# Kernel optimization log

Measured on AMD Instinct MI355X. Metric: run time of the kernel, lower is better.

The kernel has to match this reference:

```python
import jax, jax.numpy as jnp
import numpy as np

N_NODES = 100000
N_EDGES = 6400000
DIM_FEAT = 5


def setup_inputs() -> dict:
    key = jax.random.key(0)
    k1, k2, k3 = jax.random.split(key, 3)
    features = jax.random.normal(k1, (N_NODES, DIM_FEAT), dtype=jnp.float32)
    src = jax.random.randint(k2, (N_EDGES,), 0, N_NODES, dtype=jnp.int64)
    dst = jax.random.randint(k3, (N_EDGES,), 0, N_NODES, dtype=jnp.int64)
    return {"features": features, "src": src, "dst": dst}


def reference(features, src, dst):
    # copy_u('h','m') then sum('m','h'):
    # h_out[v] = sum over edges (u->v) of features[u]
    msgs = features[src]  # [E, F] gather
    h = jax.ops.segment_sum(msgs, dst, num_segments=N_NODES)  # [N, F]
    return h
```

## Files before the change

### kernel.cpp

```cpp
#include <hip/hip_runtime.h>
#include <hip/hip_bf16.h>


#define NN     100000
#define FD     5
#define NOUTT  (NN * FD)
#define NPS    128
#define NPS_SH 7
#define NB     782
#define NBP    1024
#define NSB    256
#define BLK    256

__global__ __launch_bounds__(BLK) void k1_pad(const float* __restrict__ f,
                                              float4* __restrict__ fp) {
    int i = blockIdx.x * BLK + threadIdx.x;
    if (i < NN) {
        const float* r = f + (long long)i * FD;
        fp[2 * i]     = make_float4(r[0], r[1], r[2], r[3]);
        fp[2 * i + 1] = make_float4(r[4], 0.f, 0.f, 0.f);
    }
}

__global__ __launch_bounds__(BLK) void k2_hist(const int* __restrict__ dst,
                                               int* __restrict__ blk_hist, int chunk) {
    __shared__ int h[NB];
    for (int b = threadIdx.x; b < NB; b += BLK) h[b] = 0;
    __syncthreads();
    long long e0 = (long long)blockIdx.x * chunk;
    const int4* d4 = (const int4*)(dst + e0);
    int n4 = chunk >> 2;
    for (int i = threadIdx.x; i < n4; i += BLK) {
        int4 d = d4[i];
        atomicAdd(&h[d.x >> NPS_SH], 1);
        atomicAdd(&h[d.y >> NPS_SH], 1);
        atomicAdd(&h[d.z >> NPS_SH], 1);
        atomicAdd(&h[d.w >> NPS_SH], 1);
    }
    __syncthreads();
    for (int b = threadIdx.x; b < NB; b += BLK)
        blk_hist[b * NSB + blockIdx.x] = h[b];
}

__global__ __launch_bounds__(BLK) void k3_scanblk(int* __restrict__ blk_hist,
                                                  int* __restrict__ btot) {
    __shared__ int s[BLK];
    int b = blockIdx.x, t = threadIdx.x;
    int x = blk_hist[b * NSB + t];
    s[t] = x;
    __syncthreads();
    for (int off = 1; off < BLK; off <<= 1) {
        int v = (t >= off) ? s[t - off] : 0;
        __syncthreads();
        s[t] += v;
        __syncthreads();
    }
    blk_hist[b * NSB + t] = s[t] - x;
    if (t == BLK - 1) btot[b] = s[t];
}

__global__ __launch_bounds__(BLK) void k4_scanbkt(const int* __restrict__ btot,
                                                  int* __restrict__ bbase) {
    __shared__ int s[BLK];
    int t = threadIdx.x;
    int v[4], sum = 0;
#pragma unroll
    for (int k = 0; k < 4; ++k) {
        int i = 4 * t + k;
        v[k] = (i < NB) ? btot[i] : 0;
        sum += v[k];
    }
    s[t] = sum;
    __syncthreads();
    for (int off = 1; off < BLK; off <<= 1) {
        int u = (t >= off) ? s[t - off] : 0;
        __syncthreads();
        s[t] += u;
        __syncthreads();
    }
    int run = s[t] - sum;
#pragma unroll
    for (int k = 0; k < 4; ++k) { bbase[4 * t + k] = run; run += v[k]; }
}

__global__ __launch_bounds__(BLK) void k5_scatter(const int* __restrict__ src,
                                                  const int* __restrict__ dst,
                                                  const int* __restrict__ blk_hist,
                                                  const int* __restrict__ bbase,
                                                  int* __restrict__ bdata, int chunk) {
    __shared__ int cur[NB];
    int blk = blockIdx.x;
    for (int b = threadIdx.x; b < NB; b += BLK)
        cur[b] = bbase[b] + blk_hist[b * NSB + blk];
    __syncthreads();
    long long e0 = (long long)blk * chunk;
    const int4* d4 = (const int4*)(dst + e0);
    const int4* s4 = (const int4*)(src + e0);
    int n4 = chunk >> 2;
    for (int i = threadIdx.x; i < n4; i += BLK) {
        int4 d = d4[i];
        int4 s = s4[i];
        int vv[4] = {d.x, d.y, d.z, d.w};
        int uu[4] = {s.x, s.y, s.z, s.w};
#pragma unroll
        for (int j = 0; j < 4; ++j) {
            int b = vv[j] >> NPS_SH;
            int off = atomicAdd(&cur[b], 1);
            bdata[off] = (uu[j] << NPS_SH) | (vv[j] & (NPS - 1));
        }
    }
}

__global__ __launch_bounds__(BLK) void k6_gather(const int* __restrict__ bdata,
                                                 const float4* __restrict__ fp,
                                                 const int* __restrict__ bbase,
                                                 const int* __restrict__ btot,
                                                 float* __restrict__ out) {
    __shared__ float acc[NPS * FD];
    for (int j = threadIdx.x; j < NPS * FD; j += BLK) acc[j] = 0.f;
    __syncthreads();
    int b = blockIdx.x;
    int base = bbase[b];
    int n = btot[b];
    int t = threadIdx.x;
    int i = t;
    for (; i + 3 * BLK < n; i += 4 * BLK) {
        int w0 = bdata[base + i];
        int w1 = bdata[base + i + BLK];
        int w2 = bdata[base + i + 2 * BLK];
        int w3 = bdata[base + i + 3 * BLK];
        int u0 = w0 >> NPS_SH, l0 = w0 & (NPS - 1);
        int u1 = w1 >> NPS_SH, l1 = w1 & (NPS - 1);
        int u2 = w2 >> NPS_SH, l2 = w2 & (NPS - 1);
        int u3 = w3 >> NPS_SH, l3 = w3 & (NPS - 1);
        float4 a0 = fp[2 * u0], c0 = fp[2 * u0 + 1];
        float4 a1 = fp[2 * u1], c1 = fp[2 * u1 + 1];
        float4 a2 = fp[2 * u2], c2 = fp[2 * u2 + 1];
        float4 a3 = fp[2 * u3], c3 = fp[2 * u3 + 1];
        atomicAdd(&acc[l0 * FD + 0], a0.x); atomicAdd(&acc[l0 * FD + 1], a0.y);
        atomicAdd(&acc[l0 * FD + 2], a0.z); atomicAdd(&acc[l0 * FD + 3], a0.w);
        atomicAdd(&acc[l0 * FD + 4], c0.x);
        atomicAdd(&acc[l1 * FD + 0], a1.x); atomicAdd(&acc[l1 * FD + 1], a1.y);
        atomicAdd(&acc[l1 * FD + 2], a1.z); atomicAdd(&acc[l1 * FD + 3], a1.w);
        atomicAdd(&acc[l1 * FD + 4], c1.x);
        atomicAdd(&acc[l2 * FD + 0], a2.x); atomicAdd(&acc[l2 * FD + 1], a2.y);
        atomicAdd(&acc[l2 * FD + 2], a2.z); atomicAdd(&acc[l2 * FD + 3], a2.w);
        atomicAdd(&acc[l2 * FD + 4], c2.x);
        atomicAdd(&acc[l3 * FD + 0], a3.x); atomicAdd(&acc[l3 * FD + 1], a3.y);
        atomicAdd(&acc[l3 * FD + 2], a3.z); atomicAdd(&acc[l3 * FD + 3], a3.w);
        atomicAdd(&acc[l3 * FD + 4], c3.x);
    }
    for (; i < n; i += BLK) {
        int w = bdata[base + i];
        int u = w >> NPS_SH, l = w & (NPS - 1);
        float4 a = fp[2 * u], c = fp[2 * u + 1];
        atomicAdd(&acc[l * FD + 0], a.x); atomicAdd(&acc[l * FD + 1], a.y);
        atomicAdd(&acc[l * FD + 2], a.z); atomicAdd(&acc[l * FD + 3], a.w);
        atomicAdd(&acc[l * FD + 4], c.x);
    }
    __syncthreads();
    int node0 = b * NPS;
    int nn = NN - node0; if (nn > NPS) nn = NPS;
    int nfl = nn * FD;
    float* o = out + (long long)node0 * FD;
    for (int j = t; j < nfl; j += BLK) o[j] = acc[j];
}

__global__ void scatter_add_fallback(const float* __restrict__ features,
                                     const int* __restrict__ src,
                                     const int* __restrict__ dst,
                                     float* __restrict__ out, int n_edges) {
    int idx = blockIdx.x * blockDim.x + threadIdx.x;
    int stride = gridDim.x * blockDim.x;
    for (int e = idx; e < n_edges; e += stride) {
        int u = src[e], v = dst[e];
        const float* f = features + (long long)u * FD;
        float* o = out + (long long)v * FD;
#pragma unroll
        for (int k = 0; k < FD; ++k) atomicAdd(&o[k], f[k]);
    }
}

extern "C" void kernel_launch(void* const* d_in, const int* in_sizes, int n_in,
                              void* d_out, int out_size, void* d_ws, size_t ws_size,
                              hipStream_t stream) {
    const float* features = (const float*)d_in[0];
    const int*   src      = (const int*)d_in[1];
    const int*   dst      = (const int*)d_in[2];
    float* out = (float*)d_out;
    int n_edges = in_sizes[1];

    size_t o_bd = 0;
    size_t o_fp = o_bd + (size_t)n_edges * 4;
    size_t o_bh = o_fp + (size_t)NN * 2 * sizeof(float4);
    size_t o_bb = o_bh + (size_t)NB * NSB * 4;
    size_t o_bt = o_bb + (size_t)NBP * 4;
    size_t need = o_bt + (size_t)NBP * 4;

    bool fast = (out_size == NOUTT) && (in_sizes[0] == NOUTT) &&
                (n_edges % (NSB * 4) == 0) && (need <= ws_size);

    if (fast) {
        char* w = (char*)d_ws;
        int*    bdata = (int*)(w + o_bd);
        float4* fpad  = (float4*)(w + o_fp);
        int*    bhist = (int*)(w + o_bh);
        int*    bbase = (int*)(w + o_bb);
        int*    btot  = (int*)(w + o_bt);
        int chunk = n_edges / NSB;
        k1_pad   <<<(NN + BLK - 1) / BLK, BLK, 0, stream>>>(features, fpad);
        k2_hist  <<<NSB, BLK, 0, stream>>>(dst, bhist, chunk);
        k3_scanblk<<<NB, BLK, 0, stream>>>(bhist, btot);
        k4_scanbkt<<<1,  BLK, 0, stream>>>(btot, bbase);
        k5_scatter<<<NSB, BLK, 0, stream>>>(src, dst, bhist, bbase, bdata, chunk);
        k6_gather <<<NB,  BLK, 0, stream>>>(bdata, fpad, bbase, btot, out);
    } else {
        hipMemsetAsync(d_out, 0, (size_t)out_size * sizeof(float), stream);
        int grid = (n_edges + BLK - 1) / BLK;
        if (grid > 65535) grid = 65535;
        scatter_add_fallback<<<grid, BLK, 0, stream>>>(features, src, dst, out, n_edges);
    }
}
```

Baseline: 387.7 us.

## Shrink buckets to 32 nodes, 16-bit histograms, overlap pad buffer, deeper gather unroll

Reduces bucket size from 128 to 32 nodes (3125 buckets) and doubles the number of scatter blocks to 512. Per-block histograms are stored as row-major unsigned shorts, and the scan handles two entries per thread. The padded-feature buffer now reuses the histogram workspace, with the pad kernel moved after the scatter. The gather loop is unrolled 8 deep and loads only the needed fifth float. Smaller buckets and more blocks are meant to raise gather parallelism, and the smaller histogram cuts traffic, but the scan and scatter stages carry more per-bucket overhead, and the 16-bit counts rely on per-block bucket counts fitting in 16 bits.

```diff
diff --git a/kernel.cpp b/kernel.cpp
--- a/kernel.cpp
+++ b/kernel.cpp
@@ -5,25 +5,15 @@
 #define NN     100000
 #define FD     5
 #define NOUTT  (NN * FD)
-#define NPS    128
-#define NPS_SH 7
-#define NB     782
-#define NBP    1024
-#define NSB    256
+#define NPS    32
+#define NPS_SH 5
+#define NB     3125
+#define NSB    512
 #define BLK    256
 
-__global__ __launch_bounds__(BLK) void k1_pad(const float* __restrict__ f,
-                                              float4* __restrict__ fp) {
-    int i = blockIdx.x * BLK + threadIdx.x;
-    if (i < NN) {
-        const float* r = f + (long long)i * FD;
-        fp[2 * i]     = make_float4(r[0], r[1], r[2], r[3]);
-        fp[2 * i + 1] = make_float4(r[4], 0.f, 0.f, 0.f);
-    }
-}
-
 __global__ __launch_bounds__(BLK) void k2_hist(const int* __restrict__ dst,
-                                               int* __restrict__ blk_hist, int chunk) {
+                                               unsigned short* __restrict__ bh,
+                                               int chunk) {
     __shared__ int h[NB];
     for (int b = threadIdx.x; b < NB; b += BLK) h[b] = 0;
     __syncthreads();
@@ -38,16 +28,18 @@
         atomicAdd(&h[d.w >> NPS_SH], 1);
     }
     __syncthreads();
-    for (int b = threadIdx.x; b < NB; b += BLK)
-        blk_hist[b * NSB + blockIdx.x] = h[b];
-}
-
-__global__ __launch_bounds__(BLK) void k3_scanblk(int* __restrict__ blk_hist,
+    unsigned short* row = bh + (size_t)blockIdx.x * NB;
+    for (int b = threadIdx.x; b < NB; b += BLK) row[b] = (unsigned short)h[b];
+}
+
+__global__ __launch_bounds__(BLK) void k3_scanblk(unsigned short* __restrict__ bh,
                                                   int* __restrict__ btot) {
     __shared__ int s[BLK];
     int b = blockIdx.x, t = threadIdx.x;
-    int x = blk_hist[b * NSB + t];
-    s[t] = x;
+    int v0 = bh[(size_t)(2 * t)     * NB + b];
+    int v1 = bh[(size_t)(2 * t + 1) * NB + b];
+    int pair = v0 + v1;
+    s[t] = pair;
     __syncthreads();
     for (int off = 1; off < BLK; off <<= 1) {
         int v = (t >= off) ? s[t - off] : 0;
@@ -55,18 +47,21 @@
         s[t] += v;
         __syncthreads();
     }
-    blk_hist[b * NSB + t] = s[t] - x;
+    int base = s[t] - pair;
+    bh[(size_t)(2 * t)     * NB + b] = (unsigned short)base;
+    bh[(size_t)(2 * t + 1) * NB + b] = (unsigned short)(base + v0);
     if (t == BLK - 1) btot[b] = s[t];
 }
 
+#define VPT 13
 __global__ __launch_bounds__(BLK) void k4_scanbkt(const int* __restrict__ btot,
                                                   int* __restrict__ bbase) {
     __shared__ int s[BLK];
     int t = threadIdx.x;
-    int v[4], sum = 0;
-#pragma unroll
-    for (int k = 0; k < 4; ++k) {
-        int i = 4 * t + k;
+    int v[VPT], sum = 0;
+#pragma unroll
+    for (int k = 0; k < VPT; ++k) {
+        int i = VPT * t + k;
         v[k] = (i < NB) ? btot[i] : 0;
         sum += v[k];
     }
@@ -80,18 +75,23 @@
     }
     int run = s[t] - sum;
 #pragma unroll
-    for (int k = 0; k < 4; ++k) { bbase[4 * t + k] = run; run += v[k]; }
+    for (int k = 0; k < VPT; ++k) {
+        int i = VPT * t + k;
+        if (i < NB) bbase[i] = run;
+        run += v[k];
+    }
 }
 
 __global__ __launch_bounds__(BLK) void k5_scatter(const int* __restrict__ src,
                                                   const int* __restrict__ dst,
-                                                  const int* __restrict__ blk_hist,
+                                                  const unsigned short* __restrict__ bh,
                                                   const int* __restrict__ bbase,
                                                   int* __restrict__ bdata, int chunk) {
     __shared__ int cur[NB];
     int blk = blockIdx.x;
+    const unsigned short* row = bh + (size_t)blk * NB;
     for (int b = threadIdx.x; b < NB; b += BLK)
-        cur[b] = bbase[b] + blk_hist[b * NSB + blk];
+        cur[b] = bbase[b] + (int)row[b];
     __syncthreads();
     long long e0 = (long long)blk * chunk;
     const int4* d4 = (const int4*)(dst + e0);
@@ -111,59 +111,67 @@
     }
 }
 
+__global__ __launch_bounds__(BLK) void k1_pad(const float* __restrict__ f,
+                                              float4* __restrict__ fp) {
+    int i = blockIdx.x * BLK + threadIdx.x;
+    if (i < NN) {
+        const float* r = f + (long long)i * FD;
+        fp[2 * i]     = make_float4(r[0], r[1], r[2], r[3]);
+        fp[2 * i + 1] = make_float4(r[4], 0.f, 0.f, 0.f);
+    }
+}
+
+#define UNR 8
 __global__ __launch_bounds__(BLK) void k6_gather(const int* __restrict__ bdata,
                                                  const float4* __restrict__ fp,
                                                  const int* __restrict__ bbase,
                                                  const int* __restrict__ btot,
                                                  float* __restrict__ out) {
     __shared__ float acc[NPS * FD];
-    for (int j = threadIdx.x; j < NPS * FD; j += BLK) acc[j] = 0.f;
+    int t = threadIdx.x;
+    if (t < NPS * FD) acc[t] = 0.f;
     __syncthreads();
     int b = blockIdx.x;
     int base = bbase[b];
     int n = btot[b];
-    int t = threadIdx.x;
+    const float* fpf = (const float*)fp;
+
     int i = t;
-    for (; i + 3 * BLK < n; i += 4 * BLK) {
-        int w0 = bdata[base + i];
-        int w1 = bdata[base + i + BLK];
-        int w2 = bdata[base + i + 2 * BLK];
-        int w3 = bdata[base + i + 3 * BLK];
-        int u0 = w0 >> NPS_SH, l0 = w0 & (NPS - 1);
-        int u1 = w1 >> NPS_SH, l1 = w1 & (NPS - 1);
-        int u2 = w2 >> NPS_SH, l2 = w2 & (NPS - 1);
-        int u3 = w3 >> NPS_SH, l3 = w3 & (NPS - 1);
-        float4 a0 = fp[2 * u0], c0 = fp[2 * u0 + 1];
-        float4 a1 = fp[2 * u1], c1 = fp[2 * u1 + 1];
-        float4 a2 = fp[2 * u2], c2 = fp[2 * u2 + 1];
-        float4 a3 = fp[2 * u3], c3 = fp[2 * u3 + 1];
-        atomicAdd(&acc[l0 * FD + 0], a0.x); atomicAdd(&acc[l0 * FD + 1], a0.y);
-        atomicAdd(&acc[l0 * FD + 2], a0.z); atomicAdd(&acc[l0 * FD + 3], a0.w);
-        atomicAdd(&acc[l0 * FD + 4], c0.x);
-        atomicAdd(&acc[l1 * FD + 0], a1.x); atomicAdd(&acc[l1 * FD + 1], a1.y);
-        atomicAdd(&acc[l1 * FD + 2], a1.z); atomicAdd(&acc[l1 * FD + 3], a1.w);
-        atomicAdd(&acc[l1 * FD + 4], c1.x);
-        atomicAdd(&acc[l2 * FD + 0], a2.x); atomicAdd(&acc[l2 * FD + 1], a2.y);
-        atomicAdd(&acc[l2 * FD + 2], a2.z); atomicAdd(&acc[l2 * FD + 3], a2.w);
-        atomicAdd(&acc[l2 * FD + 4], c2.x);
-        atomicAdd(&acc[l3 * FD + 0], a3.x); atomicAdd(&acc[l3 * FD + 1], a3.y);
-        atomicAdd(&acc[l3 * FD + 2], a3.z); atomicAdd(&acc[l3 * FD + 3], a3.w);
-        atomicAdd(&acc[l3 * FD + 4], c3.x);
+    for (; i + (UNR - 1) * BLK < n; i += UNR * BLK) {
+        int    l[UNR];
+        float4 a[UNR];
+        float  cx[UNR];
+#pragma unroll
+        for (int k = 0; k < UNR; ++k) {
+            int w = bdata[base + i + k * BLK];
+            int u = w >> NPS_SH;
+            l[k] = w & (NPS - 1);
+            a[k] = fp[2 * u];
+            cx[k] = fpf[8 * u + 4];
+        }
+#pragma unroll
+        for (int k = 0; k < UNR; ++k) {
+            float* p = acc + l[k] * FD;
+            atomicAdd(&p[0], a[k].x);
+            atomicAdd(&p[1], a[k].y);
+            atomicAdd(&p[2], a[k].z);
+            atomicAdd(&p[3], a[k].w);
+            atomicAdd(&p[4], cx[k]);
+        }
     }
     for (; i < n; i += BLK) {
         int w = bdata[base + i];
-        int u = w >> NPS_SH, l = w & (NPS - 1);
-        float4 a = fp[2 * u], c = fp[2 * u + 1];
-        atomicAdd(&acc[l * FD + 0], a.x); atomicAdd(&acc[l * FD + 1], a.y);
-        atomicAdd(&acc[l * FD + 2], a.z); atomicAdd(&acc[l * FD + 3], a.w);
-        atomicAdd(&acc[l * FD + 4], c.x);
-    }
-    __syncthreads();
-    int node0 = b * NPS;
-    int nn = NN - node0; if (nn > NPS) nn = NPS;
-    int nfl = nn * FD;
-    float* o = out + (long long)node0 * FD;
-    for (int j = t; j < nfl; j += BLK) o[j] = acc[j];
+        int u = w >> NPS_SH;
+        int l = w & (NPS - 1);
+        float4 a = fp[2 * u];
+        float cx = fpf[8 * u + 4];
+        float* p = acc + l * FD;
+        atomicAdd(&p[0], a.x); atomicAdd(&p[1], a.y); atomicAdd(&p[2], a.z);
+        atomicAdd(&p[3], a.w); atomicAdd(&p[4], cx);
+    }
+    __syncthreads();
+    float* o = out + (long long)b * NPS * FD;
+    if (t < NPS * FD) o[t] = acc[t];
 }
 
 __global__ void scatter_add_fallback(const float* __restrict__ features,
@@ -191,28 +199,31 @@
     int n_edges = in_sizes[1];
 
     size_t o_bd = 0;
-    size_t o_fp = o_bd + (size_t)n_edges * 4;
-    size_t o_bh = o_fp + (size_t)NN * 2 * sizeof(float4);
-    size_t o_bb = o_bh + (size_t)NB * NSB * 4;
-    size_t o_bt = o_bb + (size_t)NBP * 4;
-    size_t need = o_bt + (size_t)NBP * 4;
+    size_t o_bh = o_bd + (size_t)n_edges * 4;
+    size_t o_fp = o_bh;
+    size_t sz_overlap = (size_t)NSB * NB * 2;
+    size_t sz_fp = (size_t)NN * 2 * sizeof(float4);
+    if (sz_fp > sz_overlap) sz_overlap = sz_fp;
+    size_t o_bb = o_bh + ((sz_overlap + 15) & ~(size_t)15);
+    size_t o_bt = o_bb + (size_t)NB * 4;
+    size_t need = o_bt + (size_t)NB * 4;
 
     bool fast = (out_size == NOUTT) && (in_sizes[0] == NOUTT) &&
                 (n_edges % (NSB * 4) == 0) && (need <= ws_size);
 
     if (fast) {
         char* w = (char*)d_ws;
-        int*    bdata = (int*)(w + o_bd);
-        float4* fpad  = (float4*)(w + o_fp);
-        int*    bhist = (int*)(w + o_bh);
-        int*    bbase = (int*)(w + o_bb);
-        int*    btot  = (int*)(w + o_bt);
+        int*            bdata = (int*)(w + o_bd);
+        unsigned short* bhist = (unsigned short*)(w + o_bh);
+        float4*         fpad  = (float4*)(w + o_fp);
+        int*            bbase = (int*)(w + o_bb);
+        int*            btot  = (int*)(w + o_bt);
         int chunk = n_edges / NSB;
-        k1_pad   <<<(NN + BLK - 1) / BLK, BLK, 0, stream>>>(features, fpad);
         k2_hist  <<<NSB, BLK, 0, stream>>>(dst, bhist, chunk);
         k3_scanblk<<<NB, BLK, 0, stream>>>(bhist, btot);
         k4_scanbkt<<<1,  BLK, 0, stream>>>(btot, bbase);
         k5_scatter<<<NSB, BLK, 0, stream>>>(src, dst, bhist, bbase, bdata, chunk);
+        k1_pad   <<<(NN + BLK - 1) / BLK, BLK, 0, stream>>>(features, fpad);
         k6_gather <<<NB,  BLK, 0, stream>>>(bdata, fpad, bbase, btot, out);
     } else {
         hipMemsetAsync(d_out, 0, (size_t)out_size * sizeof(float), stream);
```

Result: no change. 394.1 us (+1.7%).
